# Optimization experiments

Measured on AMD Instinct MI355X. Metric: run time of the kernel, lower is better.

Reference implementation:

```python
import jax, jax.numpy as jnp
import numpy as np

N_ATOMS = 65536
N_SPECIES = 4
N_MOL = 512
F_PS = 512
F_MP = 256
H = 256
EPS = 1e-5


def _layer_norm(x, gamma, beta):
    mu = jnp.mean(x, axis=-1, keepdims=True)
    var = jnp.mean(jnp.square(x - mu), axis=-1, keepdims=True)
    return (x - mu) * jax.lax.rsqrt(var + EPS) * gamma + beta


def _species_mlp(x, W1, W2, W3):
    # x: [N, F], atoms grouped into S contiguous equal-size species blocks.
    S = W1.shape[0]
    N, F = x.shape
    xs = x.reshape(S, N // S, F)                       # [S, N/S, F]
    h = jax.nn.silu(jnp.einsum('snf,sfh->snh', xs, W1))  # grouped GEMM + SiLU
    h = jax.nn.silu(jnp.einsum('snh,sho->sno', h, W2))
    e = jnp.einsum('snh,sho->sno', h, W3)              # [S, N/S, 1]
    return e.reshape(N, -1)                            # keys_to_samples: back to per-atom


def setup_inputs() -> dict:
    key = jax.random.key(0)
    ks = jax.random.split(key, 10)
    inp = {
        'x_ps': jax.random.normal(ks[0], (N_ATOMS, F_PS), dtype=jnp.float32),
        'x_mp': jax.random.normal(ks[1], (N_ATOMS, F_MP), dtype=jnp.float32),
        'batch': jax.random.randint(ks[2], (N_ATOMS,), 0, N_MOL),
        'gamma_ps': jnp.ones((F_PS,), jnp.float32),
        'beta_ps': jnp.zeros((F_PS,), jnp.float32),
        'gamma_mp': jnp.ones((F_MP,), jnp.float32),
        'beta_mp': jnp.zeros((F_MP,), jnp.float32),
        'W_ps1': jax.random.normal(ks[3], (N_SPECIES, F_PS, H), jnp.float32) / np.sqrt(F_PS),
        'W_ps2': jax.random.normal(ks[4], (N_SPECIES, H, H), jnp.float32) / np.sqrt(H),
        'W_ps3': jax.random.normal(ks[5], (N_SPECIES, H, 1), jnp.float32) / np.sqrt(H),
        'W_mp1': jax.random.normal(ks[6], (N_SPECIES, F_MP, H), jnp.float32) / np.sqrt(F_MP),
        'W_mp2': jax.random.normal(ks[7], (N_SPECIES, H, H), jnp.float32) / np.sqrt(H),
        'W_mp3': jax.random.normal(ks[8], (N_SPECIES, H, 1), jnp.float32) / np.sqrt(H),
    }
    return inp


def reference(x_ps, x_mp, batch, gamma_ps, beta_ps, gamma_mp, beta_mp,
              W_ps1, W_ps2, W_ps3, W_mp1, W_mp2, W_mp3):
    norm_factor = jnp.float32(1.0)  # normalization_factor buffer
    f_ps = _layer_norm(x_ps, gamma_ps, beta_ps)
    f_mp = _layer_norm(x_mp, gamma_mp, beta_mp)
    e_ps = _species_mlp(f_ps, W_ps1, W_ps2, W_ps3)   # [N, 1] per-atom energies
    e_mp = _species_mlp(f_mp, W_mp1, W_mp2, W_mp3)   # [N, 1]
    # index_add_ scatter: per-atom -> per-molecule
    energies_ps = jax.ops.segment_sum(e_ps, batch, num_segments=N_MOL) / norm_factor
    energies_mp = jax.ops.segment_sum(e_mp, batch, num_segments=N_MOL) / norm_factor
    return energies_ps + energies_mp                 # [N_MOL, 1] (training path)
```

## Files before the change

kernel.cpp:

```cpp
#include <hip/hip_runtime.h>

#define N_ATOMS 65536
#define N_SPECIES 4
#define N_MOL 512
#define ATOMS_PER_SPECIES (N_ATOMS / N_SPECIES)

typedef __attribute__((ext_vector_type(8))) __bf16 bf16x8;
typedef __attribute__((ext_vector_type(4))) float f32x4;

__device__ __forceinline__ unsigned short f2bf(float f) {
    unsigned int u = __float_as_uint(f);
    unsigned int r = (u + 0x7fffu + ((u >> 16) & 1u)) >> 16;
    return (unsigned short)r;
}

__device__ __forceinline__ float silu(float v) {
    return v / (1.0f + __expf(-v));
}

#define WS_W1PS 0
#define WS_W2PS 524288
#define WS_W1MP 786432
#define WS_W2MP 1048576
#define WS_GB_BYTES 2621440

__global__ __launch_bounds__(256) void prep_w(const float* __restrict__ Wps1,
                                              const float* __restrict__ Wps2,
                                              const float* __restrict__ Wmp1,
                                              const float* __restrict__ Wmp2,
                                              const float* __restrict__ g_ps,
                                              const float* __restrict__ b_ps,
                                              const float* __restrict__ g_mp,
                                              const float* __restrict__ b_mp,
                                              short* __restrict__ wdst,
                                              float* __restrict__ gb) {
    __shared__ short Ts[16384];
    int b = blockIdx.x;
    const float* src; int K; long dstbase; int s, c;
    const float* ga = nullptr; const float* be = nullptr; float* gbd = nullptr;
    if (b < 32)      { src = Wps1; K = 512; s = b >> 3;        c = b & 7;        dstbase = WS_W1PS;
                       ga = g_ps; be = b_ps; gbd = gb; }
    else if (b < 48) { src = Wps2; K = 256; s = (b - 32) >> 2; c = (b - 32) & 3; dstbase = WS_W2PS; }
    else if (b < 64) { src = Wmp1; K = 256; s = (b - 48) >> 2; c = (b - 48) & 3; dstbase = WS_W1MP;
                       ga = g_mp; be = b_mp; gbd = gb + 2048; }
    else             { src = Wmp2; K = 256; s = (b - 64) >> 2; c = (b - 64) & 3; dstbase = WS_W2MP; }
    int n = threadIdx.x;
    int k0 = c * 64;
    const float* sp = src + (long)s * K * 256 + (long)k0 * 256 + n;
    float gs = 0.0f, bs = 0.0f;
    if (gbd) {
        #pragma unroll 4
        for (int kl = 0; kl < 64; ++kl) {
            float v = sp[(long)kl * 256];
            gs += ga[k0 + kl] * v;
            bs += be[k0 + kl] * v;
            Ts[(n * 64 + kl) ^ ((n & 7) << 3)] = (short)f2bf(v);
        }
        atomicAdd(&gbd[s * 256 + n], gs);
        atomicAdd(&gbd[1024 + s * 256 + n], bs);
    } else {
        #pragma unroll 4
        for (int kl = 0; kl < 64; ++kl) {
            float v = sp[(long)kl * 256];
            Ts[(n * 64 + kl) ^ ((n & 7) << 3)] = (short)f2bf(v);
        }
    }
    __syncthreads();
    long base = dstbase + (long)s * K * 256 + (long)c * 16384;
    int4* dp = (int4*)(wdst + base);
    const int4* tp = (const int4*)Ts;
    #pragma unroll
    for (int i = 0; i < 8; ++i) dp[threadIdx.x + i * 256] = tp[threadIdx.x + i * 256];
}

template <int F>
__global__ __launch_bounds__(512, 1) void mlp_kernel(
    const float* __restrict__ x, const float* __restrict__ gamma,
    const short* __restrict__ W1, const short* __restrict__ W2,
    const float* __restrict__ gW1, const float* __restrict__ bW1,
    const float* __restrict__ W3, const int* __restrict__ batch,
    float* __restrict__ out) {
    constexpr int BM = 128;
    constexpr int NCHUNK1 = F / 64;
    __shared__ short As[BM * 64];
    __shared__ short Bs[256 * 64];
    __shared__ short H1[BM * 256];
    __shared__ float2 rowstats[BM];
    __shared__ float e_lds[BM];

    const int tid = threadIdx.x;
    const int lane = tid & 63;
    const int wid = tid >> 6;
    const int wm = (wid >> 2) * 64;
    const int wn = (wid & 3) * 64;
    const int lg = lane >> 4;
    const int ln = lane & 15;

    const int block0 = blockIdx.x * BM;
    const int species = block0 / ATOMS_PER_SPECIES;
    const long wbase = (long)species * F * 256;
    const long w2base = (long)species * 256 * 256;

    if (tid < BM) { rowstats[tid] = make_float2(0.0f, 0.0f); e_lds[tid] = 0.0f; }

    f32x4 acc[4][4];
    #pragma unroll
    for (int m = 0; m < 4; ++m)
        #pragma unroll
        for (int n = 0; n < 4; ++n) acc[m][n] = (f32x4){0.f, 0.f, 0.f, 0.f};

    const int ar = tid >> 2;
    const int aj = tid & 3;
    const float* xrow = x + (long)(block0 + ar) * F;

    for (int c = 0; c < NCHUNK1; ++c) {
        __syncthreads();
        {
            int k0 = c * 64;
            float s1 = 0.0f, s2 = 0.0f;
            #pragma unroll
            for (int i = 0; i < 4; ++i) {
                int k = aj * 16 + i * 4;
                float4 xv = *(const float4*)(xrow + k0 + k);
                float4 gv = *(const float4*)(gamma + k0 + k);
                s1 += xv.x + xv.y + xv.z + xv.w;
                s2 += xv.x * xv.x + xv.y * xv.y + xv.z * xv.z + xv.w * xv.w;
                unsigned int lo = (unsigned int)f2bf(xv.x * gv.x) | ((unsigned int)f2bf(xv.y * gv.y) << 16);
                unsigned int hi = (unsigned int)f2bf(xv.z * gv.z) | ((unsigned int)f2bf(xv.w * gv.w) << 16);
                int e = (ar * 64 + k) ^ ((ar & 7) << 3);
                *(int2*)&As[e] = make_int2((int)lo, (int)hi);
            }
            s1 += __shfl_xor(s1, 1); s1 += __shfl_xor(s1, 2);
            s2 += __shfl_xor(s2, 1); s2 += __shfl_xor(s2, 2);
            if (aj == 0) {
                float2 rs = rowstats[ar];
                rs.x += s1; rs.y += s2;
                rowstats[ar] = rs;
            }
        }
        {
            const int4* src = (const int4*)(W1 + wbase + (long)c * 16384);
            int4* dst = (int4*)Bs;
            #pragma unroll
            for (int q = 0; q < 4; ++q) dst[tid + q * 512] = src[tid + q * 512];
        }
        __syncthreads();
        #pragma unroll
        for (int ks = 0; ks < 2; ++ks) {
            bf16x8 a[4], b[4];
            #pragma unroll
            for (int m = 0; m < 4; ++m) {
                int row = wm + m * 16 + ln;
                int e = (row * 64 + ks * 32 + lg * 8) ^ ((row & 7) << 3);
                a[m] = *(const bf16x8*)&As[e];
            }
            #pragma unroll
            for (int n = 0; n < 4; ++n) {
                int col = wn + n * 16 + ln;
                int e = (col * 64 + ks * 32 + lg * 8) ^ ((col & 7) << 3);
                b[n] = *(const bf16x8*)&Bs[e];
            }
            #pragma unroll
            for (int m = 0; m < 4; ++m)
                #pragma unroll
                for (int n = 0; n < 4; ++n)
                    acc[m][n] = __builtin_amdgcn_mfma_f32_16x16x32_bf16(a[m], b[n], acc[m][n], 0, 0, 0);
        }
    }

    float gw[4], bw[4], w3c[4];
    #pragma unroll
    for (int n = 0; n < 4; ++n) {
        int col = wn + n * 16 + ln;
        gw[n]  = gW1[species * 256 + col];
        bw[n]  = bW1[species * 256 + col];
        w3c[n] = W3[species * 256 + col];
    }
    const float invF = 1.0f / (float)F;
    #pragma unroll
    for (int m = 0; m < 4; ++m) {
        #pragma unroll
        for (int rr = 0; rr < 4; ++rr) {
            int row = wm + m * 16 + lg * 4 + rr;
            float2 rs = rowstats[row];
            float mu = rs.x * invF;
            float var = rs.y * invF - mu * mu;
            float rstd = rsqrtf(var + 1e-5f);
            float nmu = rstd * mu;
            #pragma unroll
            for (int n = 0; n < 4; ++n) {
                float v = rstd * acc[m][n][rr] - nmu * gw[n] + bw[n];
                float h = silu(v);
                int col = wn + n * 16 + ln;
                H1[(row * 256 + col) ^ ((row & 7) << 3)] = (short)f2bf(h);
            }
        }
    }
    __syncthreads();

    f32x4 acc2[4][4];
    #pragma unroll
    for (int m = 0; m < 4; ++m)
        #pragma unroll
        for (int n = 0; n < 4; ++n) acc2[m][n] = (f32x4){0.f, 0.f, 0.f, 0.f};

    for (int c = 0; c < 4; ++c) {
        if (c) __syncthreads();
        {
            const int4* src = (const int4*)(W2 + w2base + (long)c * 16384);
            int4* dst = (int4*)Bs;
            #pragma unroll
            for (int q = 0; q < 4; ++q) dst[tid + q * 512] = src[tid + q * 512];
        }
        __syncthreads();
        #pragma unroll
        for (int ks = 0; ks < 2; ++ks) {
            bf16x8 a[4], b[4];
            #pragma unroll
            for (int m = 0; m < 4; ++m) {
                int row = wm + m * 16 + ln;
                int e = (row * 256 + c * 64 + ks * 32 + lg * 8) ^ ((row & 7) << 3);
                a[m] = *(const bf16x8*)&H1[e];
            }
            #pragma unroll
            for (int n = 0; n < 4; ++n) {
                int col = wn + n * 16 + ln;
                int e = (col * 64 + ks * 32 + lg * 8) ^ ((col & 7) << 3);
                b[n] = *(const bf16x8*)&Bs[e];
            }
            #pragma unroll
            for (int m = 0; m < 4; ++m)
                #pragma unroll
                for (int n = 0; n < 4; ++n)
                    acc2[m][n] = __builtin_amdgcn_mfma_f32_16x16x32_bf16(a[m], b[n], acc2[m][n], 0, 0, 0);
        }
    }

    #pragma unroll
    for (int m = 0; m < 4; ++m) {
        #pragma unroll
        for (int rr = 0; rr < 4; ++rr) {
            float p = 0.0f;
            #pragma unroll
            for (int n = 0; n < 4; ++n) {
                float v = acc2[m][n][rr];
                p += silu(v) * w3c[n];
            }
            p += __shfl_xor(p, 1); p += __shfl_xor(p, 2);
            p += __shfl_xor(p, 4); p += __shfl_xor(p, 8);
            if (ln == 0) atomicAdd(&e_lds[wm + m * 16 + lg * 4 + rr], p);
        }
    }
    __syncthreads();
    if (tid < BM) {
        int mol = batch[block0 + tid];
        atomicAdd(out + mol, e_lds[tid]);
    }
}

extern "C" void kernel_launch(void* const* d_in, const int* in_sizes, int n_in,
                              void* d_out, int out_size, void* d_ws, size_t ws_size,
                              hipStream_t stream) {
    const float* x_ps     = (const float*)d_in[0];
    const float* x_mp     = (const float*)d_in[1];
    const int*   batch    = (const int*)d_in[2];
    const float* gamma_ps = (const float*)d_in[3];
    const float* beta_ps  = (const float*)d_in[4];
    const float* gamma_mp = (const float*)d_in[5];
    const float* beta_mp  = (const float*)d_in[6];
    const float* W_ps1    = (const float*)d_in[7];
    const float* W_ps2    = (const float*)d_in[8];
    const float* W_ps3    = (const float*)d_in[9];
    const float* W_mp1    = (const float*)d_in[10];
    const float* W_mp2    = (const float*)d_in[11];
    const float* W_mp3    = (const float*)d_in[12];

    float* out = (float*)d_out;
    short* wsW = (short*)d_ws;
    float* gb  = (float*)((char*)d_ws + WS_GB_BYTES);

    hipMemsetAsync(out, 0, N_MOL * sizeof(float), stream);
    hipMemsetAsync(gb, 0, 4096 * sizeof(float), stream);

    hipLaunchKernelGGL(prep_w, dim3(80), dim3(256), 0, stream,
                       W_ps1, W_ps2, W_mp1, W_mp2,
                       gamma_ps, beta_ps, gamma_mp, beta_mp, wsW, gb);

    hipLaunchKernelGGL((mlp_kernel<512>), dim3(N_ATOMS / 128), dim3(512), 0, stream,
                       x_ps, gamma_ps, wsW + WS_W1PS, wsW + WS_W2PS,
                       gb + 0, gb + 1024, W_ps3, batch, out);
    hipLaunchKernelGGL((mlp_kernel<256>), dim3(N_ATOMS / 128), dim3(512), 0, stream,
                       x_mp, gamma_mp, wsW + WS_W1MP, wsW + WS_W2MP,
                       gb + 2048, gb + 3072, W_mp3, batch, out);
}
```

Measured before the change: 180.5 us.

## Merge both MLP kernels into one smaller-tile launch with async LDS loads

Replaces the two templated 128-row, 512-thread MLP launches with a single 2048-block launch of 64-row, 256-thread tiles that handles both the ps and mp branches. This is meant to allow three blocks per CU, and the larger grid and merged launch are meant to improve latency hiding and load balance across CUs. Weight tiles are copied straight from global memory into LDS with global_load_lds using a new 32-wide K chunk swizzle, and prep_w is changed to write weights in that layout. Gamma is now folded into the bf16 W1 image instead of being multiplied into the activations per element. The cost is more reloads of the weights (each is fetched by twice as many tiles) and more barriers per chunk.

After: 147.6 us. -18.2%, faster.

```diff
diff --git a/kernel.cpp b/kernel.cpp
--- a/kernel.cpp
+++ b/kernel.cpp
@@ -1,22 +1,28 @@
 #include <hip/hip_runtime.h>
 
 #define N_ATOMS 65536
-#define N_SPECIES 4
 #define N_MOL 512
-#define ATOMS_PER_SPECIES (N_ATOMS / N_SPECIES)
 
 typedef __attribute__((ext_vector_type(8))) __bf16 bf16x8;
 typedef __attribute__((ext_vector_type(4))) float f32x4;
 
-__device__ __forceinline__ unsigned short f2bf(float f) {
+__device__ __forceinline__ unsigned int f2bf(float f) {
     unsigned int u = __float_as_uint(f);
-    unsigned int r = (u + 0x7fffu + ((u >> 16) & 1u)) >> 16;
-    return (unsigned short)r;
+    return (u + 0x7fffu + ((u >> 16) & 1u)) >> 16;
+}
+
+__device__ __forceinline__ int pack2(float a, float b) {
+    return (int)(f2bf(a) | (f2bf(b) << 16));
 }
 
 __device__ __forceinline__ float silu(float v) {
     return v / (1.0f + __expf(-v));
 }
+
+#define GLDS16(gp, lp)                                                        \
+    __builtin_amdgcn_global_load_lds(                                         \
+        (__attribute__((address_space(1))) void*)(uintptr_t)(gp),             \
+        (__attribute__((address_space(3))) void*)(uintptr_t)(lp), 16, 0, 0)
 
 #define WS_W1PS 0
 #define WS_W2PS 524288
@@ -47,22 +53,27 @@
     int n = threadIdx.x;
     int k0 = c * 64;
     const float* sp = src + (long)s * K * 256 + (long)k0 * 256 + n;
-    float gs = 0.0f, bs = 0.0f;
-    if (gbd) {
+    if (ga) {
+        float gs = 0.0f, bs = 0.0f;
         #pragma unroll 4
         for (int kl = 0; kl < 64; ++kl) {
             float v = sp[(long)kl * 256];
-            gs += ga[k0 + kl] * v;
+            unsigned int h = f2bf(v * ga[k0 + kl]);
+            gs += __uint_as_float(h << 16);
             bs += be[k0 + kl] * v;
-            Ts[(n * 64 + kl) ^ ((n & 7) << 3)] = (short)f2bf(v);
+            int klc = kl & 31, ch = kl >> 5;
+            int i16 = n * 4 + ((klc >> 3) ^ ((n >> 1) & 3));
+            Ts[ch * 8192 + i16 * 8 + (klc & 7)] = (short)h;
         }
         atomicAdd(&gbd[s * 256 + n], gs);
         atomicAdd(&gbd[1024 + s * 256 + n], bs);
     } else {
         #pragma unroll 4
         for (int kl = 0; kl < 64; ++kl) {
-            float v = sp[(long)kl * 256];
-            Ts[(n * 64 + kl) ^ ((n & 7) << 3)] = (short)f2bf(v);
+            unsigned int h = f2bf(sp[(long)kl * 256]);
+            int klc = kl & 31, ch = kl >> 5;
+            int i16 = n * 4 + ((klc >> 3) ^ ((n >> 1) & 3));
+            Ts[ch * 8192 + i16 * 8 + (klc & 7)] = (short)h;
         }
     }
     __syncthreads();
@@ -73,115 +84,111 @@
     for (int i = 0; i < 8; ++i) dp[threadIdx.x + i * 256] = tp[threadIdx.x + i * 256];
 }
 
-template <int F>
-__global__ __launch_bounds__(512, 1) void mlp_kernel(
-    const float* __restrict__ x, const float* __restrict__ gamma,
-    const short* __restrict__ W1, const short* __restrict__ W2,
-    const float* __restrict__ gW1, const float* __restrict__ bW1,
-    const float* __restrict__ W3, const int* __restrict__ batch,
-    float* __restrict__ out) {
-    constexpr int BM = 128;
-    constexpr int NCHUNK1 = F / 64;
-    __shared__ short As[BM * 64];
-    __shared__ short Bs[256 * 64];
-    __shared__ short H1[BM * 256];
-    __shared__ float2 rowstats[BM];
-    __shared__ float e_lds[BM];
+__global__ __launch_bounds__(256, 3) void mlp_all(
+    const float* __restrict__ x_ps, const float* __restrict__ x_mp,
+    const short* __restrict__ wimg, const float* __restrict__ gb,
+    const float* __restrict__ W3ps, const float* __restrict__ W3mp,
+    const int* __restrict__ batch, float* __restrict__ out) {
+    __shared__ short As[2048];
+    __shared__ short Bs[8192];
+    __shared__ short H1[16384];
+    __shared__ float2 rowstats[64];
+    __shared__ float e_lds[64];
 
     const int tid = threadIdx.x;
     const int lane = tid & 63;
     const int wid = tid >> 6;
-    const int wm = (wid >> 2) * 64;
-    const int wn = (wid & 3) * 64;
+    const int wn = wid * 64;
     const int lg = lane >> 4;
     const int ln = lane & 15;
 
-    const int block0 = blockIdx.x * BM;
-    const int species = block0 / ATOMS_PER_SPECIES;
-    const long wbase = (long)species * F * 256;
-    const long w2base = (long)species * 256 * 256;
-
-    if (tid < BM) { rowstats[tid] = make_float2(0.0f, 0.0f); e_lds[tid] = 0.0f; }
-
-    f32x4 acc[4][4];
-    #pragma unroll
-    for (int m = 0; m < 4; ++m)
-        #pragma unroll
-        for (int n = 0; n < 4; ++n) acc[m][n] = (f32x4){0.f, 0.f, 0.f, 0.f};
+    const bool mp = blockIdx.x >= 1024;
+    const int tile = mp ? (int)blockIdx.x - 1024 : (int)blockIdx.x;
+    const float* x = mp ? x_mp : x_ps;
+    const int F = mp ? 256 : 512;
+    const int nch1 = F >> 5;
+    const int block0 = tile * 64;
+    const int species = block0 >> 14;
+    const short* W1 = wimg + (mp ? WS_W1MP : WS_W1PS) + (size_t)species * F * 256;
+    const short* W2 = wimg + (mp ? WS_W2MP : WS_W2PS) + (size_t)species * 65536;
+    const float* gW1 = gb + (mp ? 2048 : 0) + species * 256;
+    const float* bW1 = gW1 + 1024;
+    const float* W3 = (mp ? W3mp : W3ps) + species * 256;
+
+    if (tid < 64) e_lds[tid] = 0.0f;
 
     const int ar = tid >> 2;
     const int aj = tid & 3;
-    const float* xrow = x + (long)(block0 + ar) * F;
-
-    for (int c = 0; c < NCHUNK1; ++c) {
+    const float* xrow = x + (size_t)(block0 + ar) * F + aj * 8;
+
+    f32x4 acc[4][4];
+    #pragma unroll
+    for (int m = 0; m < 4; ++m)
+        #pragma unroll
+        for (int n = 0; n < 4; ++n) acc[m][n] = (f32x4){0.f, 0.f, 0.f, 0.f};
+    float s1 = 0.0f, s2 = 0.0f;
+
+    for (int c = 0; c < nch1; ++c) {
+        if (c) __syncthreads();
+        {
+            const int4* gsrc = (const int4*)(W1 + (size_t)c * 8192);
+            int4* bsl = (int4*)Bs;
+            #pragma unroll
+            for (int q = 0; q < 4; ++q) {
+                int idx = wid * 256 + q * 64;
+                GLDS16(gsrc + idx + lane, bsl + idx);
+            }
+        }
+        {
+            const float4 u = *(const float4*)(xrow + c * 32);
+            const float4 v = *(const float4*)(xrow + c * 32 + 4);
+            s1 += u.x + u.y + u.z + u.w + v.x + v.y + v.z + v.w;
+            s2 += u.x * u.x + u.y * u.y + u.z * u.z + u.w * u.w
+                + v.x * v.x + v.y * v.y + v.z * v.z + v.w * v.w;
+            int4 p;
+            p.x = pack2(u.x, u.y); p.y = pack2(u.z, u.w);
+            p.z = pack2(v.x, v.y); p.w = pack2(v.z, v.w);
+            int i16 = ar * 4 + (aj ^ ((ar >> 1) & 3));
+            *(int4*)&As[i16 * 8] = p;
+        }
         __syncthreads();
-        {
-            int k0 = c * 64;
-            float s1 = 0.0f, s2 = 0.0f;
-            #pragma unroll
-            for (int i = 0; i < 4; ++i) {
-                int k = aj * 16 + i * 4;
-                float4 xv = *(const float4*)(xrow + k0 + k);
-                float4 gv = *(const float4*)(gamma + k0 + k);
-                s1 += xv.x + xv.y + xv.z + xv.w;
-                s2 += xv.x * xv.x + xv.y * xv.y + xv.z * xv.z + xv.w * xv.w;
-                unsigned int lo = (unsigned int)f2bf(xv.x * gv.x) | ((unsigned int)f2bf(xv.y * gv.y) << 16);
-                unsigned int hi = (unsigned int)f2bf(xv.z * gv.z) | ((unsigned int)f2bf(xv.w * gv.w) << 16);
-                int e = (ar * 64 + k) ^ ((ar & 7) << 3);
-                *(int2*)&As[e] = make_int2((int)lo, (int)hi);
-            }
-            s1 += __shfl_xor(s1, 1); s1 += __shfl_xor(s1, 2);
-            s2 += __shfl_xor(s2, 1); s2 += __shfl_xor(s2, 2);
-            if (aj == 0) {
-                float2 rs = rowstats[ar];
-                rs.x += s1; rs.y += s2;
-                rowstats[ar] = rs;
-            }
-        }
-        {
-            const int4* src = (const int4*)(W1 + wbase + (long)c * 16384);
-            int4* dst = (int4*)Bs;
-            #pragma unroll
-            for (int q = 0; q < 4; ++q) dst[tid + q * 512] = src[tid + q * 512];
-        }
-        __syncthreads();
-        #pragma unroll
-        for (int ks = 0; ks < 2; ++ks) {
-            bf16x8 a[4], b[4];
-            #pragma unroll
-            for (int m = 0; m < 4; ++m) {
-                int row = wm + m * 16 + ln;
-                int e = (row * 64 + ks * 32 + lg * 8) ^ ((row & 7) << 3);
-                a[m] = *(const bf16x8*)&As[e];
-            }
-            #pragma unroll
-            for (int n = 0; n < 4; ++n) {
-                int col = wn + n * 16 + ln;
-                int e = (col * 64 + ks * 32 + lg * 8) ^ ((col & 7) << 3);
-                b[n] = *(const bf16x8*)&Bs[e];
-            }
-            #pragma unroll
-            for (int m = 0; m < 4; ++m)
-                #pragma unroll
-                for (int n = 0; n < 4; ++n)
-                    acc[m][n] = __builtin_amdgcn_mfma_f32_16x16x32_bf16(a[m], b[n], acc[m][n], 0, 0, 0);
-        }
-    }
-
-    float gw[4], bw[4], w3c[4];
+        bf16x8 a[4], b[4];
+        #pragma unroll
+        for (int m = 0; m < 4; ++m) {
+            int row = m * 16 + ln;
+            int i16 = row * 4 + (lg ^ ((row >> 1) & 3));
+            a[m] = *(const bf16x8*)&As[i16 * 8];
+        }
+        #pragma unroll
+        for (int n = 0; n < 4; ++n) {
+            int col = wn + n * 16 + ln;
+            int i16 = col * 4 + (lg ^ ((col >> 1) & 3));
+            b[n] = *(const bf16x8*)&Bs[i16 * 8];
+        }
+        #pragma unroll
+        for (int m = 0; m < 4; ++m)
+            #pragma unroll
+            for (int n = 0; n < 4; ++n)
+                acc[m][n] = __builtin_amdgcn_mfma_f32_16x16x32_bf16(a[m], b[n], acc[m][n], 0, 0, 0);
+    }
+
+    s1 += __shfl_xor(s1, 1); s1 += __shfl_xor(s1, 2);
+    s2 += __shfl_xor(s2, 1); s2 += __shfl_xor(s2, 2);
+    if (aj == 0) rowstats[ar] = make_float2(s1, s2);
+    __syncthreads();
+
+    float gwv[4], bwv[4], w3v[4];
     #pragma unroll
     for (int n = 0; n < 4; ++n) {
         int col = wn + n * 16 + ln;
-        gw[n]  = gW1[species * 256 + col];
-        bw[n]  = bW1[species * 256 + col];
-        w3c[n] = W3[species * 256 + col];
-    }
-    const float invF = 1.0f / (float)F;
+        gwv[n] = gW1[col]; bwv[n] = bW1[col]; w3v[n] = W3[col];
+    }
+    const float invF = mp ? (1.0f / 256.0f) : (1.0f / 512.0f);
     #pragma unroll
     for (int m = 0; m < 4; ++m) {
         #pragma unroll
         for (int rr = 0; rr < 4; ++rr) {
-            int row = wm + m * 16 + lg * 4 + rr;
+            int row = m * 16 + lg * 4 + rr;
             float2 rs = rowstats[row];
             float mu = rs.x * invF;
             float var = rs.y * invF - mu * mu;
@@ -189,14 +196,12 @@
             float nmu = rstd * mu;
             #pragma unroll
             for (int n = 0; n < 4; ++n) {
-                float v = rstd * acc[m][n][rr] - nmu * gw[n] + bw[n];
-                float h = silu(v);
+                float v = rstd * acc[m][n][rr] - nmu * gwv[n] + bwv[n];
                 int col = wn + n * 16 + ln;
-                H1[(row * 256 + col) ^ ((row & 7) << 3)] = (short)f2bf(h);
+                H1[(row * 256 + col) ^ ((row & 7) << 3)] = (short)f2bf(silu(v));
             }
         }
     }
-    __syncthreads();
 
     f32x4 acc2[4][4];
     #pragma unroll
@@ -204,58 +209,53 @@
         #pragma unroll
         for (int n = 0; n < 4; ++n) acc2[m][n] = (f32x4){0.f, 0.f, 0.f, 0.f};
 
-    for (int c = 0; c < 4; ++c) {
-        if (c) __syncthreads();
+    for (int c = 0; c < 8; ++c) {
+        __syncthreads();
         {
-            const int4* src = (const int4*)(W2 + w2base + (long)c * 16384);
-            int4* dst = (int4*)Bs;
-            #pragma unroll
-            for (int q = 0; q < 4; ++q) dst[tid + q * 512] = src[tid + q * 512];
+            const int4* gsrc = (const int4*)(W2 + (size_t)c * 8192);
+            int4* bsl = (int4*)Bs;
+            #pragma unroll
+            for (int q = 0; q < 4; ++q) {
+                int idx = wid * 256 + q * 64;
+                GLDS16(gsrc + idx + lane, bsl + idx);
+            }
         }
         __syncthreads();
-        #pragma unroll
-        for (int ks = 0; ks < 2; ++ks) {
-            bf16x8 a[4], b[4];
-            #pragma unroll
-            for (int m = 0; m < 4; ++m) {
-                int row = wm + m * 16 + ln;
-                int e = (row * 256 + c * 64 + ks * 32 + lg * 8) ^ ((row & 7) << 3);
-                a[m] = *(const bf16x8*)&H1[e];
-            }
-            #pragma unroll
-            for (int n = 0; n < 4; ++n) {
-                int col = wn + n * 16 + ln;
-                int e = (col * 64 + ks * 32 + lg * 8) ^ ((col & 7) << 3);
-                b[n] = *(const bf16x8*)&Bs[e];
-            }
-            #pragma unroll
-            for (int m = 0; m < 4; ++m)
-                #pragma unroll
-                for (int n = 0; n < 4; ++n)
-                    acc2[m][n] = __builtin_amdgcn_mfma_f32_16x16x32_bf16(a[m], b[n], acc2[m][n], 0, 0, 0);
-        }
+        bf16x8 a[4], b[4];
+        #pragma unroll
+        for (int m = 0; m < 4; ++m) {
+            int row = m * 16 + ln;
+            int e = (row * 256 + c * 32 + lg * 8) ^ ((row & 7) << 3);
+            a[m] = *(const bf16x8*)&H1[e];
+        }
+        #pragma unroll
+        for (int n = 0; n < 4; ++n) {
+            int col = wn + n * 16 + ln;
+            int i16 = col * 4 + (lg ^ ((col >> 1) & 3));
+            b[n] = *(const bf16x8*)&Bs[i16 * 8];
+        }
+        #pragma unroll
+        for (int m = 0; m < 4; ++m)
+            #pragma unroll
+            for (int n = 0; n < 4; ++n)
+                acc2[m][n] = __builtin_amdgcn_mfma_f32_16x16x32_bf16(a[m], b[n], acc2[m][n], 0, 0, 0);
     }
 
     #pragma unroll
     for (int m = 0; m < 4; ++m) {
         #pragma unroll
         for (int rr = 0; rr < 4; ++rr) {
+            int row = m * 16 + lg * 4 + rr;
             float p = 0.0f;
             #pragma unroll
-            for (int n = 0; n < 4; ++n) {
-                float v = acc2[m][n][rr];
-                p += silu(v) * w3c[n];
-            }
+            for (int n = 0; n < 4; ++n) p += silu(acc2[m][n][rr]) * w3v[n];
             p += __shfl_xor(p, 1); p += __shfl_xor(p, 2);
             p += __shfl_xor(p, 4); p += __shfl_xor(p, 8);
-            if (ln == 0) atomicAdd(&e_lds[wm + m * 16 + lg * 4 + rr], p);
+            if (ln == 0) atomicAdd(&e_lds[row], p);
         }
     }
     __syncthreads();
-    if (tid < BM) {
-        int mol = batch[block0 + tid];
-        atomicAdd(out + mol, e_lds[tid]);
-    }
+    if (tid < 64) atomicAdd(out + batch[block0 + tid], e_lds[tid]);
 }
 
 extern "C" void kernel_launch(void* const* d_in, const int* in_sizes, int n_in,
@@ -286,10 +286,6 @@
                        W_ps1, W_ps2, W_mp1, W_mp2,
                        gamma_ps, beta_ps, gamma_mp, beta_mp, wsW, gb);
 
-    hipLaunchKernelGGL((mlp_kernel<512>), dim3(N_ATOMS / 128), dim3(512), 0, stream,
-                       x_ps, gamma_ps, wsW + WS_W1PS, wsW + WS_W2PS,
-                       gb + 0, gb + 1024, W_ps3, batch, out);
-    hipLaunchKernelGGL((mlp_kernel<256>), dim3(N_ATOMS / 128), dim3(512), 0, stream,
-                       x_mp, gamma_mp, wsW + WS_W1MP, wsW + WS_W2MP,
-                       gb + 2048, gb + 3072, W_mp3, batch, out);
-}
+    hipLaunchKernelGGL(mlp_all, dim3(2048), dim3(256), 0, stream,
+                       x_ps, x_mp, wsW, gb, W_ps3, W_mp3, batch, out);
+}
```
